# Performance work log

Measured on AMD Instinct MI355X. Metric: run time of the kernel, lower is better.

## Reference

```python
import jax, jax.numpy as jnp
import numpy as np

GROUPS = 32  # min(32, 256//4)
EPS = 1e-5


def setup_inputs() -> dict:
    key = jax.random.key(0)
    ks = jax.random.split(key, 4)
    B, C, H, W = 8, 256, 128, 128
    x = jax.random.normal(ks[0], (B, C, H, W), dtype=jnp.float32)
    gn_w = jnp.ones((C,), dtype=jnp.float32)
    gn_b = jnp.zeros((C,), dtype=jnp.float32)
    qkv_w = jax.random.normal(ks[1], (3 * C, C), dtype=jnp.float32) * (C ** -0.5)
    qkv_b = jnp.zeros((3 * C,), dtype=jnp.float32)
    proj_w = jax.random.normal(ks[2], (C, C), dtype=jnp.float32) * (C ** -0.5)
    proj_b = jnp.zeros((C,), dtype=jnp.float32)
    return {"x": x, "gn_w": gn_w, "gn_b": gn_b, "qkv_w": qkv_w,
            "qkv_b": qkv_b, "proj_w": proj_w, "proj_b": proj_b}


def _group_norm(x, w, b):
    B, C, H, W = x.shape
    xg = x.reshape(B, GROUPS, C // GROUPS, H, W)
    mean = xg.mean(axis=(2, 3, 4), keepdims=True)
    var = xg.var(axis=(2, 3, 4), keepdims=True)
    xg = (xg - mean) * jax.lax.rsqrt(var + EPS)
    x = xg.reshape(B, C, H, W)
    return x * w[None, :, None, None] + b[None, :, None, None]


def reference(x, gn_w, gn_b, qkv_w, qkv_b, proj_w, proj_b):
    B, C, H, W = x.shape
    num_heads = 8
    head_dim = C // num_heads
    scale = head_dim ** -0.5

    h = _group_norm(x, gn_w, gn_b)
    # 1x1 conv == per-pixel matmul over channels
    qkv = jnp.einsum('bchw,oc->bohw', h, qkv_w) + qkv_b[None, :, None, None]
    qkv = qkv.reshape(B, 3, num_heads, head_dim, H * W)
    q, k, v = qkv[:, 0], qkv[:, 1], qkv[:, 2]  # each (B, h, head_dim, HW)
    # Faithful to source: contracts over spatial axis d=HW -> (B,h,hd,hd)
    attn = jnp.einsum('bhid,bhjd->bhij', q, k) * scale
    attn = jax.nn.softmax(attn, axis=-1)
    out = jnp.einsum('bhij,bhjd->bhid', attn, v)  # (B, h, head_dim, HW)
    out = out.reshape(B, C, H, W)
    out = jnp.einsum('bchw,oc->bohw', out, proj_w) + proj_b[None, :, None, None]
    return x + out
```

## Files before the change

### kernel.cpp

```cpp
#include <hip/hip_runtime.h>
#include <stdint.h>

typedef __bf16 bf16;
typedef __attribute__((ext_vector_type(8))) __bf16 bf16x8;
typedef __attribute__((ext_vector_type(4))) float f32x4;

#define S_HW 16384
#define N_C 256

__device__ __forceinline__ f32x4 mfma16(bf16x8 a, bf16x8 b, f32x4 c) {
  return __builtin_amdgcn_mfma_f32_16x16x32_bf16(a, b, c, 0, 0, 0);
}
__device__ __forceinline__ void async_ld16(const bf16* g, bf16* l) {
  __builtin_amdgcn_global_load_lds(
      (const __attribute__((address_space(1))) unsigned int*)g,
      (__attribute__((address_space(3))) unsigned int*)l, 16, 0, 0);
}
__device__ __forceinline__ unsigned short bf2u(bf16 h) {
  union { bf16 h; unsigned short u; } c; c.h = h; return c.u;
}
__device__ __forceinline__ bf16 u2bf(unsigned short u) {
  union { unsigned short u; bf16 h; } c; c.u = u; return c.h;
}

__global__ __launch_bounds__(256) void k_split(
    const float* __restrict__ x, bf16* __restrict__ yhi, bf16* __restrict__ ylo,
    bf16* __restrict__ yt, float* __restrict__ Sx) {
  int b = blockIdx.z, c0 = blockIdx.y * 64, s0 = blockIdx.x * 64;
  __shared__ unsigned T[64][65];
  __shared__ float sxl[256];
  int t = threadIdx.x;
  int cl = t >> 2, sg = t & 3;
  size_t off = (size_t)(b * N_C + c0 + cl) * S_HW + s0 + sg * 16;
  const float* xp = x + off;
  bf16x8 hv[2], lv[2];
  float sum = 0.f;
#pragma unroll
  for (int i2 = 0; i2 < 4; i2++) {
    float4 v = *(const float4*)(xp + i2 * 4);
    float f4[4] = {v.x, v.y, v.z, v.w};
#pragma unroll
    for (int k = 0; k < 4; k++) {
      int i = i2 * 4 + k;
      float fv = f4[k];
      bf16 h = (bf16)fv;
      bf16 l = (bf16)(fv - (float)h);
      hv[i >> 3][i & 7] = h;
      lv[i >> 3][i & 7] = l;
      sum += fv;
      T[sg * 16 + i][cl] = (unsigned)bf2u(h) | ((unsigned)bf2u(l) << 16);
    }
  }
  *(bf16x8*)(yhi + off) = hv[0];
  *(bf16x8*)(yhi + off + 8) = hv[1];
  *(bf16x8*)(ylo + off) = lv[0];
  *(bf16x8*)(ylo + off + 8) = lv[1];
  sxl[t] = sum;
  __syncthreads();
  if (t < 64) {
    float s2 = sxl[t * 4] + sxl[t * 4 + 1] + sxl[t * 4 + 2] + sxl[t * 4 + 3];
    atomicAdd(&Sx[b * N_C + c0 + t], s2);
  }
  int sl = t >> 2, cg = t & 3;
  bf16x8 ho[2], lo2[2];
#pragma unroll
  for (int i = 0; i < 16; i++) {
    unsigned u = T[sl][cg * 16 + i];
    ho[i >> 3][i & 7] = u2bf((unsigned short)(u & 0xffffu));
    lo2[i >> 3][i & 7] = u2bf((unsigned short)(u >> 16));
  }
  size_t tb = (size_t)(b * S_HW + s0 + sl) * 512 + c0 + cg * 16;
  *(bf16x8*)(yt + tb) = ho[0];
  *(bf16x8*)(yt + tb + 8) = ho[1];
  *(bf16x8*)(yt + tb + 256) = lo2[0];
  *(bf16x8*)(yt + tb + 256 + 8) = lo2[1];
}

__global__ __launch_bounds__(256) void k_gram(
    const bf16* __restrict__ yhi, const bf16* __restrict__ ylo,
    float* __restrict__ YG3) {
  constexpr int BK = 32;
  __shared__ __align__(16) bf16 As[2][128 * BK];
  __shared__ __align__(16) bf16 Bs[2][128 * BK];
  int kc = blockIdx.x * 2048;
  int m0 = (blockIdx.y >> 2) * 128, n0 = (blockIdx.y & 3) * 128;
  int b = blockIdx.z;
  int tid = threadIdx.x, lane = tid & 63, wave = tid >> 6;
  int wm = (wave >> 1) * 64, wn = (wave & 1) * 64;
  const bf16* Ab = yhi + (size_t)(b * N_C + m0) * S_HW;
  const bf16* Bb = (n0 < 256) ? yhi + (size_t)(b * N_C + n0) * S_HW
                              : ylo + (size_t)(b * N_C + n0 - 256) * S_HW;
  f32x4 acc[4][4] = {};

  auto STAGE = [&](int buf, int kt) {
#pragma unroll
    for (int i = 0; i < 2; i++) {
      int ch = i * 256 + tid;
      int row = ch >> 2, col = (ch & 3) * 8;
      async_ld16(Ab + (size_t)row * S_HW + kt + col,
                 &As[buf][(i * 256 + wave * 64) * 8]);
      async_ld16(Bb + (size_t)row * S_HW + kt + col,
                 &Bs[buf][(i * 256 + wave * 64) * 8]);
    }
  };

  STAGE(0, kc);
  __syncthreads();
  int cur = 0;
  for (int kt = kc; kt < kc + 2048; kt += BK) {
    if (kt + BK < kc + 2048) STAGE(cur ^ 1, kt + BK);
    bf16x8 af[4], bfr[4];
    int fm = lane & 15, fk = (lane >> 4) * 8;
#pragma unroll
    for (int q = 0; q < 4; q++) {
      af[q] = *(const bf16x8*)(&As[cur][(wm + q * 16 + fm) * BK + fk]);
      bfr[q] = *(const bf16x8*)(&Bs[cur][(wn + q * 16 + fm) * BK + fk]);
    }
#pragma unroll
    for (int ti = 0; ti < 4; ti++)
#pragma unroll
      for (int tj = 0; tj < 4; tj++)
        acc[ti][tj] = mfma16(af[ti], bfr[tj], acc[ti][tj]);
    __syncthreads();
    cur ^= 1;
  }
  int quad = lane >> 4, cn = lane & 15;
#pragma unroll
  for (int ti = 0; ti < 4; ti++)
#pragma unroll
    for (int r = 0; r < 4; r++) {
      int m = m0 + wm + ti * 16 + quad * 4 + r;
#pragma unroll
      for (int tj = 0; tj < 4; tj++) {
        int n = n0 + wn + tj * 16 + cn;
        atomicAdd(&YG3[(size_t)(b * N_C + m) * 512 + n], acc[ti][tj][r]);
      }
    }
}

__global__ __launch_bounds__(256) void k_wkt(const float* __restrict__ qkv_w,
                                             float* __restrict__ WkT) {
  int k = blockIdx.x, j = threadIdx.x;
  WkT[k * 256 + j] = qkv_w[(256 + j) * 256 + k];
}

__global__ __launch_bounds__(256) void k_coefs(
    const float* __restrict__ Sx, const float* __restrict__ YG3,
    const float* __restrict__ gn_w, const float* __restrict__ gn_b,
    const float* __restrict__ qkv_w, const float* __restrict__ qkv_b,
    float* __restrict__ a_, float* __restrict__ bv_, float* __restrict__ u_,
    float* __restrict__ vbe) {
  int b = blockIdx.x, t = threadIdx.x;
  __shared__ float sxl[256], gxd[256], gm[32], gr[32], sh[256], bl[256];
  sxl[t] = Sx[b * N_C + t];
  gxd[t] = YG3[(size_t)(b * N_C + t) * 512 + t] +
           2.f * YG3[(size_t)(b * N_C + t) * 512 + 256 + t];
  __syncthreads();
  if (t < 32) {
    float s = 0.f, q2 = 0.f;
#pragma unroll
    for (int i = 0; i < 8; i++) { s += sxl[t * 8 + i]; q2 += gxd[t * 8 + i]; }
    float mean = s * (1.f / 131072.f);
    float var = q2 * (1.f / 131072.f) - mean * mean;
    gm[t] = mean;
    gr[t] = 1.f / sqrtf(var + 1e-5f);
  }
  __syncthreads();
  {
    float A = gn_w[t] * gr[t >> 3];
    float B = gn_b[t] - gm[t >> 3] * A;
    a_[b * N_C + t] = A;
    bv_[b * N_C + t] = B;
    bl[t] = B;
    sh[t] = A * sxl[t] + 16384.f * B;
  }
  __syncthreads();
  for (int r = t; r < 512; r += 256) {
    const float* wp = qkv_w + (size_t)r * 256;
    float acc = 0.f;
    for (int c = 0; c < 256; c++) acc += wp[c] * sh[c];
    u_[b * 512 + r] = acc;
  }
  {
    const float* wp = qkv_w + (size_t)(512 + t) * 256;
    float acc = 0.f;
    for (int c = 0; c < 256; c++) acc += wp[c] * bl[c];
    vbe[b * N_C + t] = acc + qkv_b[512 + t];
  }
}

__global__ __launch_bounds__(256) void k_t1(
    const float* __restrict__ YG3, const float* __restrict__ WkT,
    const float* __restrict__ a_, const float* __restrict__ bv_,
    const float* __restrict__ Sx, float* __restrict__ T1) {
  int tile = blockIdx.x, b = blockIdx.y;
  int i0 = (tile >> 2) * 64, j0 = (tile & 3) * 64;
  __shared__ float As[64][69];
  __shared__ float Bs[64][69];
  __shared__ float al[256], bl[256], sxl[256];
  int t = threadIdx.x;
  al[t] = a_[b * N_C + t];
  bl[t] = bv_[b * N_C + t];
  sxl[t] = Sx[b * N_C + t];
  int cl = t >> 2, qq = (t & 3) * 16;
  int kk = t >> 2, jj = (t & 3) * 16;
  int ti = t >> 4, tj = t & 15;
  float acc[4][4] = {};
  for (int kc = 0; kc < 256; kc += 64) {
    {
      const float* yg = YG3 + (size_t)(b * N_C + i0 + cl) * 512 + kc + qq;
#pragma unroll
      for (int i = 0; i < 16; i++) As[cl][qq + i] = yg[i] + yg[256 + i];
    }
    __syncthreads();
    {
      int cp = kc + kk;
      const float* ygp = YG3 + (size_t)(b * N_C + cp) * 512 + 256 + i0 + jj;
#pragma unroll
      for (int i = 0; i < 16; i++) As[jj + i][kk] += ygp[i];
    }
    __syncthreads();
    {
      int c = i0 + cl;
      float ac = al[c], bc = bl[c], sxc = sxl[c];
#pragma unroll
      for (int i = 0; i < 16; i++) {
        int cp = kc + qq + i;
        As[cl][qq + i] = ac * al[cp] * As[cl][qq + i] + ac * bl[cp] * sxc +
                         bc * al[cp] * sxl[cp] + 16384.f * bc * bl[cp];
      }
    }
    {
      const float* wp = WkT + (size_t)(kc + kk) * 256 + j0 + jj;
#pragma unroll
      for (int i = 0; i < 16; i += 4) {
        float4 v = *(const float4*)(wp + i);
        Bs[kk][jj + i] = v.x; Bs[kk][jj + i + 1] = v.y;
        Bs[kk][jj + i + 2] = v.z; Bs[kk][jj + i + 3] = v.w;
      }
    }
    __syncthreads();
    for (int k = 0; k < 64; k++) {
      float av[4], bv4[4];
#pragma unroll
      for (int ii = 0; ii < 4; ii++) av[ii] = As[ti * 4 + ii][k];
#pragma unroll
      for (int j2 = 0; j2 < 4; j2++) bv4[j2] = Bs[k][tj * 4 + j2];
#pragma unroll
      for (int ii = 0; ii < 4; ii++)
#pragma unroll
        for (int j2 = 0; j2 < 4; j2++) acc[ii][j2] += av[ii] * bv4[j2];
    }
    __syncthreads();
  }
#pragma unroll
  for (int ii = 0; ii < 4; ii++)
#pragma unroll
    for (int j2 = 0; j2 < 4; j2++)
      T1[(size_t)(b * N_C + i0 + ti * 4 + ii) * 256 + j0 + tj * 4 + j2] =
          acc[ii][j2];
}

__global__ __launch_bounds__(256) void k_logits(
    const float* __restrict__ T1, const float* __restrict__ qkv_w,
    const float* __restrict__ qkv_b, const float* __restrict__ u_,
    float* __restrict__ attn) {
  int h = blockIdx.x, b = blockIdx.y;
  __shared__ float Tc[64][33];
  __shared__ float Wql[32][65];
  __shared__ float Ll[32][33];
  __shared__ float uq[32], uk[32], bq[32], bk[32];
  int t = threadIdx.x;
  if (t < 32) {
    uq[t] = u_[b * 512 + h * 32 + t];
    uk[t] = u_[b * 512 + 256 + h * 32 + t];
    bq[t] = qkv_b[h * 32 + t];
    bk[t] = qkv_b[256 + h * 32 + t];
  }
  int i = t & 31, jg = t >> 5;
  float acc[4] = {};
  for (int cc = 0; cc < 256; cc += 64) {
    {
      int c_l = t >> 2, seg = (t & 3) * 8;
      const float* tp = T1 + (size_t)(b * N_C + cc + c_l) * 256 + h * 32 + seg;
      float4 v0 = *(const float4*)tp, v1 = *(const float4*)(tp + 4);
      Tc[c_l][seg] = v0.x; Tc[c_l][seg + 1] = v0.y;
      Tc[c_l][seg + 2] = v0.z; Tc[c_l][seg + 3] = v0.w;
      Tc[c_l][seg + 4] = v1.x; Tc[c_l][seg + 5] = v1.y;
      Tc[c_l][seg + 6] = v1.z; Tc[c_l][seg + 7] = v1.w;
      int row = t >> 3, seg2 = (t & 7) * 8;
      const float* wp = qkv_w + (size_t)(h * 32 + row) * 256 + cc + seg2;
      float4 w0 = *(const float4*)wp, w1 = *(const float4*)(wp + 4);
      Wql[row][seg2] = w0.x; Wql[row][seg2 + 1] = w0.y;
      Wql[row][seg2 + 2] = w0.z; Wql[row][seg2 + 3] = w0.w;
      Wql[row][seg2 + 4] = w1.x; Wql[row][seg2 + 5] = w1.y;
      Wql[row][seg2 + 6] = w1.z; Wql[row][seg2 + 7] = w1.w;
    }
    __syncthreads();
    for (int c = 0; c < 64; c++) {
      float w = Wql[i][c];
#pragma unroll
      for (int j2 = 0; j2 < 4; j2++) acc[j2] += w * Tc[c][jg * 4 + j2];
    }
    __syncthreads();
  }
  const float scale = 0.17677669529663687f;
#pragma unroll
  for (int j2 = 0; j2 < 4; j2++) {
    int j = jg * 4 + j2;
    Ll[i][j] = scale * (acc[j2] + bq[i] * uk[j] + bk[j] * uq[i] +
                        16384.f * bq[i] * bk[j]);
  }
  __syncthreads();
  if (t < 32) {
    float m = -1e30f;
    for (int j = 0; j < 32; j++) m = fmaxf(m, Ll[t][j]);
    float e[32], s = 0.f;
    for (int j = 0; j < 32; j++) { e[j] = expf(Ll[t][j] - m); s += e[j]; }
    float inv = 1.f / s;
    float* ap = attn + (size_t)((b * 8 + h) * 32 + t) * 32;
    for (int j = 0; j < 32; j++) ap[j] = e[j] * inv;
  }
}

__global__ __launch_bounds__(256) void k_m1(const float* __restrict__ proj_w,
                                            const float* __restrict__ attn,
                                            float* __restrict__ M1) {
  int o = blockIdx.x, b = blockIdx.y, t = threadIdx.x;
  __shared__ float at[8192];
  __shared__ float pl[256];
  for (int k = 0; k < 8192; k += 256) at[k + t] = attn[(size_t)b * 8192 + k + t];
  pl[t] = proj_w[(size_t)o * 256 + t];
  __syncthreads();
  int h = t >> 5, j = t & 31;
  float acc = 0.f;
#pragma unroll
  for (int i = 0; i < 32; i++) acc += pl[h * 32 + i] * at[h * 1024 + i * 32 + j];
  M1[(size_t)(b * N_C + o) * 256 + t] = acc;
}

__global__ __launch_bounds__(256) void k_m2(const float* __restrict__ M1,
                                            const float* __restrict__ qkv_w,
                                            float* __restrict__ M2) {
  int tile = blockIdx.x, b = blockIdx.y;
  int i0 = (tile >> 2) * 64, j0 = (tile & 3) * 64;
  __shared__ float As[64][69];
  __shared__ float Bs[64][69];
  int t = threadIdx.x;
  int cl = t >> 2, qq = (t & 3) * 16;
  int kk = t >> 2, jj = (t & 3) * 16;
  int ti = t >> 4, tj = t & 15;
  float acc[4][4] = {};
  for (int kc = 0; kc < 256; kc += 64) {
    {
      const float* mp = M1 + (size_t)(b * N_C + i0 + cl) * 256 + kc + qq;
#pragma unroll
      for (int i = 0; i < 16; i += 4) {
        float4 v = *(const float4*)(mp + i);
        As[cl][qq + i] = v.x; As[cl][qq + i + 1] = v.y;
        As[cl][qq + i + 2] = v.z; As[cl][qq + i + 3] = v.w;
      }
      const float* wp = qkv_w + (size_t)(512 + kc + kk) * 256 + j0 + jj;
#pragma unroll
      for (int i = 0; i < 16; i += 4) {
        float4 v = *(const float4*)(wp + i);
        Bs[kk][jj + i] = v.x; Bs[kk][jj + i + 1] = v.y;
        Bs[kk][jj + i + 2] = v.z; Bs[kk][jj + i + 3] = v.w;
      }
    }
    __syncthreads();
    for (int k = 0; k < 64; k++) {
      float av[4], bv4[4];
#pragma unroll
      for (int ii = 0; ii < 4; ii++) av[ii] = As[ti * 4 + ii][k];
#pragma unroll
      for (int j2 = 0; j2 < 4; j2++) bv4[j2] = Bs[k][tj * 4 + j2];
#pragma unroll
      for (int ii = 0; ii < 4; ii++)
#pragma unroll
        for (int j2 = 0; j2 < 4; j2++) acc[ii][j2] += av[ii] * bv4[j2];
    }
    __syncthreads();
  }
#pragma unroll
  for (int ii = 0; ii < 4; ii++)
#pragma unroll
    for (int j2 = 0; j2 < 4; j2++)
      M2[(size_t)(b * N_C + i0 + ti * 4 + ii) * 256 + j0 + tj * 4 + j2] =
          acc[ii][j2];
}

__global__ __launch_bounds__(256) void k_fa(
    const float* __restrict__ M2, const float* __restrict__ M1,
    const float* __restrict__ a_, const float* __restrict__ vbe,
    const float* __restrict__ proj_b, bf16* __restrict__ FA,
    float* __restrict__ g_) {
  int o = blockIdx.x, b = blockIdx.y, t = threadIdx.x;
  float f = M2[(size_t)(b * N_C + o) * 256 + t] * a_[b * N_C + t] +
            (t == o ? 1.0f : 0.0f);
  bf16 hi = (bf16)f;
  bf16 lo = (bf16)(f - (float)hi);
  FA[(size_t)(b * N_C + o) * 512 + t] = hi;
  FA[(size_t)(b * N_C + o) * 512 + 256 + t] = lo;
  __shared__ float red[256];
  red[t] = M1[(size_t)(b * N_C + o) * 256 + t] * vbe[b * N_C + t];
  __syncthreads();
  for (int s2 = 128; s2 > 0; s2 >>= 1) {
    if (t < s2) red[t] += red[t + s2];
    __syncthreads();
  }
  if (t == 0) g_[b * N_C + o] = red[0] + proj_b[o];
}

__global__ __launch_bounds__(256) void k_final(
    const bf16* __restrict__ FA, const bf16* __restrict__ yt,
    const float* __restrict__ g_, float* __restrict__ out) {
  constexpr int BK = 32;
  __shared__ __align__(16) bf16 As[2][128 * BK];
  __shared__ __align__(16) bf16 Bs[2][128 * BK];
  int b = blockIdx.z, m0 = blockIdx.y * 128, n0 = blockIdx.x * 128;
  int tid = threadIdx.x, lane = tid & 63, wave = tid >> 6;
  int wm = (wave >> 1) * 64, wn = (wave & 1) * 64;
  const bf16* Ab = FA + (size_t)(b * N_C + m0) * 512;
  const bf16* Bb = yt + (size_t)(b * S_HW + n0) * 512;
  f32x4 acc[4][4] = {};

  auto STAGE = [&](int buf, int kt) {
    int ka = (kt < 512) ? kt : kt - 512;
    int kb = (kt < 256) ? kt : kt - 256;
#pragma unroll
    for (int i = 0; i < 2; i++) {
      int ch = i * 256 + tid;
      int row = ch >> 2, col = (ch & 3) * 8;
      async_ld16(Ab + (size_t)row * 512 + ka + col,
                 &As[buf][(i * 256 + wave * 64) * 8]);
      async_ld16(Bb + (size_t)row * 512 + kb + col,
                 &Bs[buf][(i * 256 + wave * 64) * 8]);
    }
  };

  STAGE(0, 0);
  __syncthreads();
  int cur = 0;
  for (int kt = 0; kt < 768; kt += BK) {
    if (kt + BK < 768) STAGE(cur ^ 1, kt + BK);
    bf16x8 af[4], bfr[4];
    int fm = lane & 15, fk = (lane >> 4) * 8;
#pragma unroll
    for (int q = 0; q < 4; q++) {
      af[q] = *(const bf16x8*)(&As[cur][(wm + q * 16 + fm) * BK + fk]);
      bfr[q] = *(const bf16x8*)(&Bs[cur][(wn + q * 16 + fm) * BK + fk]);
    }
#pragma unroll
    for (int ti = 0; ti < 4; ti++)
#pragma unroll
      for (int tj = 0; tj < 4; tj++)
        acc[ti][tj] = mfma16(af[ti], bfr[tj], acc[ti][tj]);
    __syncthreads();
    cur ^= 1;
  }
  int quad = lane >> 4, cn = lane & 15;
#pragma unroll
  for (int ti = 0; ti < 4; ti++)
#pragma unroll
    for (int r = 0; r < 4; r++) {
      int row = m0 + wm + ti * 16 + quad * 4 + r;
      float gb = g_[b * N_C + row];
#pragma unroll
      for (int tj = 0; tj < 4; tj++) {
        int col = n0 + wn + tj * 16 + cn;
        size_t idx = (size_t)(b * N_C + row) * S_HW + col;
        out[idx] = acc[ti][tj][r] + gb;
      }
    }
}

extern "C" void kernel_launch(void* const* d_in, const int* in_sizes, int n_in,
                              void* d_out, int out_size, void* d_ws,
                              size_t ws_size, hipStream_t stream) {
  const float* x = (const float*)d_in[0];
  const float* gn_w = (const float*)d_in[1];
  const float* gn_b = (const float*)d_in[2];
  const float* qkv_w = (const float*)d_in[3];
  const float* qkv_b = (const float*)d_in[4];
  const float* proj_w = (const float*)d_in[5];
  const float* proj_b = (const float*)d_in[6];
  float* out = (float*)d_out;

  const size_t MB = 1ull << 20;
  char* ws = (char*)d_ws;
  bf16* ylo = (bf16*)ws;
  bf16* yt = (bf16*)(ws + 64 * MB);
  float* YG3 = (float*)(ws + 192 * MB);
  float* M1 = (float*)(ws + 192 * MB);
  bf16* FA = (bf16*)(ws + 194 * MB);
  float* WkT = (float*)(ws + 196 * MB);
  float* attn = (float*)(ws + 196 * MB + 256 * 1024);
  float* Sx = (float*)(ws + 196 * MB + 512 * 1024);
  float* a_ = (float*)(ws + 196 * MB + 520 * 1024);
  float* bv_ = (float*)(ws + 196 * MB + 528 * 1024);
  float* u_ = (float*)(ws + 196 * MB + 536 * 1024);
  float* vbe = (float*)(ws + 196 * MB + 552 * 1024);
  float* g_ = (float*)(ws + 196 * MB + 560 * 1024);
  float* T1 = (float*)(ws + 198 * MB);
  float* M2 = T1;
  bf16* yhi = (bf16*)d_out;

  if (ws_size < 200 * MB) return;

  hipMemsetAsync(YG3, 0, 4 * MB, stream);
  hipMemsetAsync(Sx, 0, 8 * 1024, stream);
  k_split<<<dim3(256, 4, 8), 256, 0, stream>>>(x, yhi, ylo, yt, Sx);
  k_gram<<<dim3(8, 8, 8), 256, 0, stream>>>(yhi, ylo, YG3);
  k_wkt<<<256, 256, 0, stream>>>(qkv_w, WkT);
  k_coefs<<<8, 256, 0, stream>>>(Sx, YG3, gn_w, gn_b, qkv_w, qkv_b, a_, bv_,
                                 u_, vbe);
  k_t1<<<dim3(16, 8), 256, 0, stream>>>(YG3, WkT, a_, bv_, Sx, T1);
  k_logits<<<dim3(8, 8), 256, 0, stream>>>(T1, qkv_w, qkv_b, u_, attn);
  k_m1<<<dim3(256, 8), 256, 0, stream>>>(proj_w, attn, M1);
  k_m2<<<dim3(16, 8), 256, 0, stream>>>(M1, qkv_w, M2);
  k_fa<<<dim3(256, 8), 256, 0, stream>>>(M2, M1, a_, vbe, proj_b, FA, g_);
  k_final<<<dim3(128, 2, 8), 256, 0, stream>>>(FA, yt, g_, out);
}
```

Measured before the change: 540.4 us.

## Triple-buffer LDS pipeline in gram and final GEMM kernels with explicit waitcnt

Replaces the double-buffered async global-to-LDS staging in k_gram and k_final with a three-stage ring buffer that prefetches two tiles ahead. Explicit vmcnt/lgkmcnt waits and raw s_barrier calls replace the per-iteration __syncthreads, so the next load is issued right after the fragments are read and overlaps the MFMA work. The aim is to hide global memory latency better in these bandwidth-heavy GEMMs. In exchange it uses 50% more LDS per block, which may reduce occupancy, and the hand-tuned vmcnt counts must match the number of loads issued per stage.

```diff
diff --git a/kernel.cpp b/kernel.cpp
--- a/kernel.cpp
+++ b/kernel.cpp
@@ -80,8 +80,10 @@
     const bf16* __restrict__ yhi, const bf16* __restrict__ ylo,
     float* __restrict__ YG3) {
   constexpr int BK = 32;
-  __shared__ __align__(16) bf16 As[2][128 * BK];
-  __shared__ __align__(16) bf16 Bs[2][128 * BK];
+  constexpr int NT = 64;
+  constexpr int BUF = 128 * BK;
+  __shared__ __align__(16) bf16 As[3 * BUF];
+  __shared__ __align__(16) bf16 Bs[3 * BUF];
   int kc = blockIdx.x * 2048;
   int m0 = (blockIdx.y >> 2) * 128, n0 = (blockIdx.y & 3) * 128;
   int b = blockIdx.z;
@@ -91,38 +93,68 @@
   const bf16* Bb = (n0 < 256) ? yhi + (size_t)(b * N_C + n0) * S_HW
                               : ylo + (size_t)(b * N_C + n0 - 256) * S_HW;
   f32x4 acc[4][4] = {};
-
-  auto STAGE = [&](int buf, int kt) {
+  int fm = lane & 15, fk = (lane >> 4) * 8;
+
+  auto STAGE = [&](int bi, int t) {
+    int kt = kc + t * BK;
 #pragma unroll
     for (int i = 0; i < 2; i++) {
       int ch = i * 256 + tid;
       int row = ch >> 2, col = (ch & 3) * 8;
       async_ld16(Ab + (size_t)row * S_HW + kt + col,
-                 &As[buf][(i * 256 + wave * 64) * 8]);
+                 As + bi * BUF + (i * 256 + wave * 64) * 8);
       async_ld16(Bb + (size_t)row * S_HW + kt + col,
-                 &Bs[buf][(i * 256 + wave * 64) * 8]);
+                 Bs + bi * BUF + (i * 256 + wave * 64) * 8);
     }
   };
 
-  STAGE(0, kc);
-  __syncthreads();
-  int cur = 0;
-  for (int kt = kc; kt < kc + 2048; kt += BK) {
-    if (kt + BK < kc + 2048) STAGE(cur ^ 1, kt + BK);
+  STAGE(0, 0);
+  STAGE(1, 1);
+  STAGE(2, 2);
+  int bi = 0;
+  for (int t = 0; t < NT - 2; t++) {
+    asm volatile("s_waitcnt vmcnt(8)" ::: "memory");
+    __builtin_amdgcn_s_barrier();
+    const bf16* Ap = As + bi * BUF;
+    const bf16* Bp = Bs + bi * BUF;
     bf16x8 af[4], bfr[4];
-    int fm = lane & 15, fk = (lane >> 4) * 8;
 #pragma unroll
     for (int q = 0; q < 4; q++) {
-      af[q] = *(const bf16x8*)(&As[cur][(wm + q * 16 + fm) * BK + fk]);
-      bfr[q] = *(const bf16x8*)(&Bs[cur][(wn + q * 16 + fm) * BK + fk]);
-    }
+      af[q] = *(const bf16x8*)(Ap + (wm + q * 16 + fm) * BK + fk);
+      bfr[q] = *(const bf16x8*)(Bp + (wn + q * 16 + fm) * BK + fk);
+    }
+    asm volatile("s_waitcnt lgkmcnt(0)" ::: "memory");
+    __builtin_amdgcn_sched_barrier(0);
+    __builtin_amdgcn_s_barrier();
+    if (t + 3 < NT) STAGE(bi, t + 3);
 #pragma unroll
     for (int ti = 0; ti < 4; ti++)
 #pragma unroll
       for (int tj = 0; tj < 4; tj++)
         acc[ti][tj] = mfma16(af[ti], bfr[tj], acc[ti][tj]);
-    __syncthreads();
-    cur ^= 1;
+    bi = (bi == 2) ? 0 : bi + 1;
+  }
+#pragma unroll
+  for (int pe = 0; pe < 2; pe++) {
+    if (pe == 0)
+      asm volatile("s_waitcnt vmcnt(4)" ::: "memory");
+    else
+      asm volatile("s_waitcnt vmcnt(0)" ::: "memory");
+    __builtin_amdgcn_s_barrier();
+    const bf16* Ap = As + bi * BUF;
+    const bf16* Bp = Bs + bi * BUF;
+    bf16x8 af[4], bfr[4];
+#pragma unroll
+    for (int q = 0; q < 4; q++) {
+      af[q] = *(const bf16x8*)(Ap + (wm + q * 16 + fm) * BK + fk);
+      bfr[q] = *(const bf16x8*)(Bp + (wn + q * 16 + fm) * BK + fk);
+    }
+#pragma unroll
+    for (int ti = 0; ti < 4; ti++)
+#pragma unroll
+      for (int tj = 0; tj < 4; tj++)
+        acc[ti][tj] = mfma16(af[ti], bfr[tj], acc[ti][tj]);
+    bi = (bi == 2) ? 0 : bi + 1;
   }
   int quad = lane >> 4, cn = lane & 15;
 #pragma unroll
@@ -416,16 +448,20 @@
     const bf16* __restrict__ FA, const bf16* __restrict__ yt,
     const float* __restrict__ g_, float* __restrict__ out) {
   constexpr int BK = 32;
-  __shared__ __align__(16) bf16 As[2][128 * BK];
-  __shared__ __align__(16) bf16 Bs[2][128 * BK];
+  constexpr int NT = 24;
+  constexpr int BUF = 128 * BK;
+  __shared__ __align__(16) bf16 As[3 * BUF];
+  __shared__ __align__(16) bf16 Bs[3 * BUF];
   int b = blockIdx.z, m0 = blockIdx.y * 128, n0 = blockIdx.x * 128;
   int tid = threadIdx.x, lane = tid & 63, wave = tid >> 6;
   int wm = (wave >> 1) * 64, wn = (wave & 1) * 64;
   const bf16* Ab = FA + (size_t)(b * N_C + m0) * 512;
   const bf16* Bb = yt + (size_t)(b * S_HW + n0) * 512;
   f32x4 acc[4][4] = {};
-
-  auto STAGE = [&](int buf, int kt) {
+  int fm = lane & 15, fk = (lane >> 4) * 8;
+
+  auto STAGE = [&](int bi, int t) {
+    int kt = t * BK;
     int ka = (kt < 512) ? kt : kt - 512;
     int kb = (kt < 256) ? kt : kt - 256;
 #pragma unroll
@@ -433,31 +469,59 @@
       int ch = i * 256 + tid;
       int row = ch >> 2, col = (ch & 3) * 8;
       async_ld16(Ab + (size_t)row * 512 + ka + col,
-                 &As[buf][(i * 256 + wave * 64) * 8]);
+                 As + bi * BUF + (i * 256 + wave * 64) * 8);
       async_ld16(Bb + (size_t)row * 512 + kb + col,
-                 &Bs[buf][(i * 256 + wave * 64) * 8]);
+                 Bs + bi * BUF + (i * 256 + wave * 64) * 8);
     }
   };
 
   STAGE(0, 0);
-  __syncthreads();
-  int cur = 0;
-  for (int kt = 0; kt < 768; kt += BK) {
-    if (kt + BK < 768) STAGE(cur ^ 1, kt + BK);
+  STAGE(1, 1);
+  STAGE(2, 2);
+  int bi = 0;
+  for (int t = 0; t < NT - 2; t++) {
+    asm volatile("s_waitcnt vmcnt(8)" ::: "memory");
+    __builtin_amdgcn_s_barrier();
+    const bf16* Ap = As + bi * BUF;
+    const bf16* Bp = Bs + bi * BUF;
     bf16x8 af[4], bfr[4];
-    int fm = lane & 15, fk = (lane >> 4) * 8;
 #pragma unroll
     for (int q = 0; q < 4; q++) {
-      af[q] = *(const bf16x8*)(&As[cur][(wm + q * 16 + fm) * BK + fk]);
-      bfr[q] = *(const bf16x8*)(&Bs[cur][(wn + q * 16 + fm) * BK + fk]);
-    }
+      af[q] = *(const bf16x8*)(Ap + (wm + q * 16 + fm) * BK + fk);
+      bfr[q] = *(const bf16x8*)(Bp + (wn + q * 16 + fm) * BK + fk);
+    }
+    asm volatile("s_waitcnt lgkmcnt(0)" ::: "memory");
+    __builtin_amdgcn_sched_barrier(0);
+    __builtin_amdgcn_s_barrier();
+    if (t + 3 < NT) STAGE(bi, t + 3);
 #pragma unroll
     for (int ti = 0; ti < 4; ti++)
 #pragma unroll
       for (int tj = 0; tj < 4; tj++)
         acc[ti][tj] = mfma16(af[ti], bfr[tj], acc[ti][tj]);
-    __syncthreads();
-    cur ^= 1;
+    bi = (bi == 2) ? 0 : bi + 1;
+  }
+#pragma unroll
+  for (int pe = 0; pe < 2; pe++) {
+    if (pe == 0)
+      asm volatile("s_waitcnt vmcnt(4)" ::: "memory");
+    else
+      asm volatile("s_waitcnt vmcnt(0)" ::: "memory");
+    __builtin_amdgcn_s_barrier();
+    const bf16* Ap = As + bi * BUF;
+    const bf16* Bp = Bs + bi * BUF;
+    bf16x8 af[4], bfr[4];
+#pragma unroll
+    for (int q = 0; q < 4; q++) {
+      af[q] = *(const bf16x8*)(Ap + (wm + q * 16 + fm) * BK + fk);
+      bfr[q] = *(const bf16x8*)(Bp + (wn + q * 16 + fm) * BK + fk);
+    }
+#pragma unroll
+    for (int ti = 0; ti < 4; ti++)
+#pragma unroll
+      for (int tj = 0; tj < 4; tj++)
+        acc[ti][tj] = mfma16(af[ti], bfr[tj], acc[ti][tj]);
+    bi = (bi == 2) ? 0 : bi + 1;
   }
   int quad = lane >> 4, cn = lane & 15;
 #pragma unroll
```

After: 539.1 us. Within noise of the previous version (-0.2%).
